# Performance work log

Hardware: AMD Instinct MI355X
Metric: run time of the kernel (lower is better)

Reference implementation:

```python
import jax, jax.numpy as jnp
import numpy as np

N, C, H, W = 10, 512, 40, 40
HW = H * W
OUT_CH = 128
EPS = 1e-12

def _l2norm(x, axis):
    # matches F.normalize: v / max(||v||_2, eps)
    n = jnp.sqrt(jnp.sum(x * x, axis=axis, keepdims=True))
    return x / jnp.maximum(n, EPS)

def _conv(x, w, b, pad):
    y = jax.lax.conv_general_dilated(
        x, w, window_strides=(1, 1), padding=[(pad, pad), (pad, pad)],
        dimension_numbers=('NCHW', 'OIHW', 'NCHW'))
    return y + b[None, :, None, None]

def setup_inputs() -> dict:
    key = jax.random.key(0)
    ks = jax.random.split(key, 6)
    feats = jax.random.normal(ks[0], (N, C, H, W), jnp.float32)
    SISMs = jax.random.uniform(ks[1], (N, 1, H, W), jnp.float32)
    # ResNetBlock(HW -> 128) params (Kaiming-uniform-ish fan-in bounds)
    s1 = float(1.0 / np.sqrt(HW * 9))
    s2 = float(1.0 / np.sqrt(OUT_CH * 9))
    ss = float(1.0 / np.sqrt(HW))
    w1 = jax.random.uniform(ks[2], (OUT_CH, HW, 3, 3), jnp.float32, -s1, s1)
    b1 = jnp.zeros((OUT_CH,), jnp.float32)
    w2 = jax.random.uniform(ks[3], (OUT_CH, OUT_CH, 3, 3), jnp.float32, -s2, s2)
    b2 = jnp.zeros((OUT_CH,), jnp.float32)
    ws = jax.random.uniform(ks[4], (OUT_CH, HW, 1, 1), jnp.float32, -ss, ss)
    bs = jnp.zeros((OUT_CH,), jnp.float32)
    return dict(feats=feats, SISMs=SISMs, w1=w1, b1=b1, w2=w2, b2=b2, ws=ws, bs=bs)

def reference(feats, SISMs, w1, b1, w2, b2, ws, bs):
    # SISMs supplied at (H,W): bilinear resize w/ align_corners=True at same size is identity
    NFs = _l2norm(feats, axis=1)                                   # (N,C,H,W)
    SIVs = _l2norm(jnp.mean(NFs * SISMs, axis=(-1, -2)), axis=1)   # (N,C)
    # CFM: 1x1 conv of NFs with SIVs as filters -> (N,N,H,W)
    cm = jnp.einsum('nchw,mc->nmhw', NFs, SIVs).reshape(N, N, HW)
    cm = _l2norm(cm, axis=2)
    corr = jnp.einsum('nmk,npk->nmp', cm, cm)                      # (N,N,N)
    wv = jax.nn.softmax(jnp.sum(corr, axis=2), axis=1)             # (N,N)
    CSA = jnp.sum(cm * wv[:, :, None], axis=1)                     # (N,HW)
    mn = jnp.min(CSA, axis=1, keepdims=True)
    mx = jnp.max(CSA, axis=1, keepdims=True)
    CSA = (CSA - mn) / (mx - mn + EPS)
    CSA_maps = CSA.reshape(N, 1, H, W)
    # self-correlation features: (N, HW, H, W)
    NFf = NFs.reshape(N, C, HW)
    SCFs = jnp.einsum('nci,ncj->nij', NFf, NFf).reshape(N, HW, H, W)
    # reorder channels by descending CSA evidence
    idx = jnp.argsort(-CSA, axis=1)                                # (N,HW)
    RSCFs = jnp.take_along_axis(SCFs, idx[:, :, None, None], axis=1)
    x = RSCFs * CSA_maps
    # ResNetBlock: relu(conv2(relu(conv1(x))) + shortcut_1x1(x))
    h = jax.nn.relu(_conv(x, w1, b1, 1))
    h = _conv(h, w2, b2, 1)
    sc = _conv(x, ws, bs, 0)
    return jax.nn.relu(h + sc)
```

## Files before the change

### kernel.cpp

```cpp
#include <hip/hip_runtime.h>
#include <hip/hip_bf16.h>
#include <math.h>

typedef short short8 __attribute__((ext_vector_type(8)));
typedef short short4v __attribute__((ext_vector_type(4)));
typedef float f32x4 __attribute__((ext_vector_type(4)));
typedef __hip_bfloat16 bf16;

#define KN 10
#define KC 512
#define KHW 1600
#define KH 40
#define KOC 128
#define KPW 42
#define KM 1280

__device__ __forceinline__ void gload16(const void* g, void* l) {
  __builtin_amdgcn_global_load_lds(
      (const __attribute__((address_space(1))) unsigned int*)g,
      (__attribute__((address_space(3))) unsigned int*)l, 16, 0, 0);
}

__device__ __forceinline__ double blockReduceSumD(double v) {
  __shared__ double tmpS[8];
  int lane = threadIdx.x & 63, wv = threadIdx.x >> 6;
  #pragma unroll
  for (int o = 32; o > 0; o >>= 1) v += __shfl_down(v, o);
  if (lane == 0) tmpS[wv] = v;
  __syncthreads();
  if (threadIdx.x == 0) {
    int nw = (blockDim.x + 63) >> 6;
    double s = 0;
    for (int i = 0; i < nw; i++) s += tmpS[i];
    tmpS[0] = s;
  }
  __syncthreads();
  double r = tmpS[0];
  __syncthreads();
  return r;
}

__device__ __forceinline__ double blockReduceMinD(double v) {
  __shared__ double tmpMn[8];
  int lane = threadIdx.x & 63, wv = threadIdx.x >> 6;
  #pragma unroll
  for (int o = 32; o > 0; o >>= 1) v = fmin(v, __shfl_down(v, o));
  if (lane == 0) tmpMn[wv] = v;
  __syncthreads();
  if (threadIdx.x == 0) {
    int nw = (blockDim.x + 63) >> 6;
    double s = tmpMn[0];
    for (int i = 1; i < nw; i++) s = fmin(s, tmpMn[i]);
    tmpMn[0] = s;
  }
  __syncthreads();
  double r = tmpMn[0];
  __syncthreads();
  return r;
}

__device__ __forceinline__ double blockReduceMaxD(double v) {
  __shared__ double tmpMx[8];
  int lane = threadIdx.x & 63, wv = threadIdx.x >> 6;
  #pragma unroll
  for (int o = 32; o > 0; o >>= 1) v = fmax(v, __shfl_down(v, o));
  if (lane == 0) tmpMx[wv] = v;
  __syncthreads();
  if (threadIdx.x == 0) {
    int nw = (blockDim.x + 63) >> 6;
    double s = tmpMx[0];
    for (int i = 1; i < nw; i++) s = fmax(s, tmpMx[i]);
    tmpMx[0] = s;
  }
  __syncthreads();
  double r = tmpMx[0];
  __syncthreads();
  return r;
}


__global__ void k_rnormp(const float* __restrict__ feats, double* __restrict__ ps) {
  int t = blockIdx.x * 256 + threadIdx.x;
  if (t >= KN * KHW) return;
  int ci = blockIdx.y;
  int n = t / KHW, k = t % KHW;
  const float* p = feats + (size_t)n * KC * KHW + (size_t)ci * 128 * KHW + k;
  double s = 0.0;
  for (int c = 0; c < 128; ++c) { double v = p[(size_t)c * KHW]; s += v * v; }
  ps[(size_t)ci * KN * KHW + t] = s;
}

__global__ void k_rnormc(const double* __restrict__ ps, double* __restrict__ rnorm) {
  int t = blockIdx.x * 256 + threadIdx.x;
  if (t >= KN * KHW) return;
  double s = ps[t] + ps[KN * KHW + t] + ps[2 * KN * KHW + t] + ps[3 * KN * KHW + t];
  double nn = sqrt(s);
  if (nn < 1e-12) nn = 1e-12;
  rnorm[t] = 1.0 / nn;
}

__global__ void k_nft(const float* __restrict__ feats, const double* __restrict__ rnorm,
                      const float* __restrict__ sism, bf16* __restrict__ NFT,
                      double* __restrict__ vpp) {
  __shared__ float T[32][33];
  int n = blockIdx.z, k0 = blockIdx.x * 32, c0 = blockIdx.y * 32;
  int tx = threadIdx.x, ty = threadIdx.y;
  const float* fb = feats + ((size_t)n * KC + c0) * KHW + k0;
  #pragma unroll
  for (int ii = 0; ii < 4; ii++) {
    int cl = ty * 4 + ii;
    T[cl][tx] = fb[(size_t)cl * KHW + tx];
  }
  __syncthreads();
  bf16* ob = NFT + ((size_t)n * KHW + k0) * KC + c0;
  #pragma unroll
  for (int ii = 0; ii < 4; ii++) {
    int kl = ty * 4 + ii;
    float r = (float)rnorm[n * KHW + k0 + kl];
    ob[(size_t)kl * KC + tx] = __float2bfloat16(T[tx][kl] * r);
  }
  double rs = rnorm[n * KHW + k0 + tx] * (double)sism[n * KHW + k0 + tx];
  #pragma unroll
  for (int ii = 0; ii < 4; ii++) {
    int cl = ty * 4 + ii;
    double v = (double)T[cl][tx] * rs;
    #pragma unroll
    for (int o = 16; o > 0; o >>= 1) v += __shfl_down(v, o, 32);
    if (tx == 0) vpp[((size_t)n * KC + c0 + cl) * 50 + k0 / 32] = v;
  }
}

__global__ void k_sivnorm2(const double* __restrict__ vpp, double* __restrict__ SIV) {
  int n = blockIdx.x, c = threadIdx.x;
  const double* p = vpp + ((size_t)n * KC + c) * 50;
  double acc = 0;
  #pragma unroll 5
  for (int j = 0; j < 50; j++) acc += p[j];
  acc /= (double)KHW;
  double s2 = blockReduceSumD(acc * acc);
  double nn = sqrt(s2);
  if (nn < 1e-12) nn = 1e-12;
  SIV[n * KC + c] = acc / nn;
}

__global__ void k_cmP(const float* __restrict__ feats, const double* __restrict__ SIV,
                      double* __restrict__ cmp) {
  __shared__ double sv[KN][64];
  int kc = blockIdx.x, ci = blockIdx.y, n = blockIdx.z;
  for (int t = threadIdx.x; t < KN * 64; t += 256) {
    int m = t / 64, c = t % 64;
    sv[m][c] = SIV[m * KC + ci * 64 + c];
  }
  __syncthreads();
  int k = kc * 256 + threadIdx.x;
  if (k >= KHW) return;
  const float* f = feats + ((size_t)n * KC + ci * 64) * KHW + k;
  double acc[KN];
  #pragma unroll
  for (int m = 0; m < KN; m++) acc[m] = 0.0;
  for (int c = 0; c < 64; ++c) {
    double fv = f[(size_t)c * KHW];
    #pragma unroll
    for (int m = 0; m < KN; m++) acc[m] += fv * sv[m][c];
  }
  const size_t str = (size_t)KN * KN * KHW;
  #pragma unroll
  for (int m = 0; m < KN; m++)
    cmp[(size_t)ci * str + ((size_t)n * KN + m) * KHW + k] = acc[m];
}

__global__ void k_cmB(const double* __restrict__ cmp, const double* __restrict__ rnorm,
                      double* __restrict__ cm) {
  size_t t = (size_t)blockIdx.x * 256 + threadIdx.x;
  if (t >= (size_t)KN * KN * KHW) return;
  int k = t % KHW;
  int n = (int)(t / ((size_t)KN * KHW));
  const size_t str = (size_t)KN * KN * KHW;
  double s = 0;
  #pragma unroll
  for (int ci = 0; ci < 8; ci++) s += cmp[ci * str + t];
  cm[t] = s * rnorm[n * KHW + k];
}

__global__ void k_cmnorm(double* __restrict__ cm) {
  double* row = cm + (size_t)blockIdx.x * KHW;
  double s = 0;
  for (int k = threadIdx.x; k < KHW; k += 256) { double v = row[k]; s += v * v; }
  s = blockReduceSumD(s);
  double nn = sqrt(s);
  if (nn < 1e-12) nn = 1e-12;
  double rn = 1.0 / nn;
  for (int k = threadIdx.x; k < KHW; k += 256) row[k] *= rn;
}

__global__ void k_st(const double* __restrict__ cm, double* __restrict__ tbuf) {
  int b = blockIdx.x;
  int n = b / KN, m = b % KN;
  const double* base = cm + (size_t)n * KN * KHW;
  double acc = 0;
  for (int k = threadIdx.x; k < KHW; k += 256) {
    double S = 0;
    #pragma unroll
    for (int mm = 0; mm < KN; mm++) S += base[(size_t)mm * KHW + k];
    acc += base[(size_t)m * KHW + k] * S;
  }
  acc = blockReduceSumD(acc);
  if (threadIdx.x == 0) tbuf[b] = acc;
}

__global__ void k_csa(const double* __restrict__ cm, const double* __restrict__ tbuf,
                      double* __restrict__ CSAd, float* __restrict__ CSAf) {
  __shared__ double w[KN];
  int n = blockIdx.x, tid = threadIdx.x;
  if (tid == 0) {
    double v[KN], mx = -1e300;
    #pragma unroll
    for (int m = 0; m < KN; m++) { v[m] = tbuf[n * KN + m]; mx = fmax(mx, v[m]); }
    double s = 0;
    #pragma unroll
    for (int m = 0; m < KN; m++) { v[m] = exp(v[m] - mx); s += v[m]; }
    #pragma unroll
    for (int m = 0; m < KN; m++) w[m] = v[m] / s;
  }
  __syncthreads();
  double v[7];
  int cnt = 0;
  double lmin = 1e300, lmax = -1e300;
  for (int k = tid; k < KHW; k += 256) {
    double a = 0;
    #pragma unroll
    for (int m = 0; m < KN; m++) a += cm[((size_t)n * KN + m) * KHW + k] * w[m];
    v[cnt++] = a;
    lmin = fmin(lmin, a);
    lmax = fmax(lmax, a);
  }
  double mn = blockReduceMinD(lmin);
  double mx = blockReduceMaxD(lmax);
  double inv = 1.0 / (mx - mn + 1e-12);
  cnt = 0;
  for (int k = tid; k < KHW; k += 256) {
    double nv = (v[cnt++] - mn) * inv;
    CSAd[(size_t)n * KHW + k] = nv;
    CSAf[(size_t)n * KHW + k] = (float)nv;
  }
}

__global__ void k_rank(const double* __restrict__ CSAd, int* __restrict__ idx) {
  __shared__ double key[KHW];
  int b = blockIdx.x;
  int n = b / 100, it = b % 100;
  const double* src = CSAd + (size_t)n * KHW;
  for (int j = threadIdx.x; j < KHW; j += 256) key[j] = src[j];
  __syncthreads();
  int wave = threadIdx.x >> 6, lane = threadIdx.x & 63;
  int i0 = it * 16 + wave * 4;
  double ki[4];
  #pragma unroll
  for (int ii = 0; ii < 4; ii++) ki[ii] = key[i0 + ii];
  int r[4] = {0, 0, 0, 0};
  #pragma unroll
  for (int q = 0; q < 25; q++) {
    int j = q * 64 + lane;
    double kj = key[j];
    #pragma unroll
    for (int ii = 0; ii < 4; ii++) {
      int i = i0 + ii;
      r[ii] += (kj > ki[ii]) || (kj == ki[ii] && j < i);
    }
  }
  #pragma unroll
  for (int ii = 0; ii < 4; ii++) {
    int v = r[ii];
    #pragma unroll
    for (int o = 32; o > 0; o >>= 1) v += __shfl_down(v, o);
    if (lane == 0) idx[n * KHW + v] = i0 + ii;
  }
}

__global__ void k_prepw1s(const float* __restrict__ w1, const float* __restrict__ wsc,
                          bf16* __restrict__ w1s) {
  int t = blockIdx.x * 256 + threadIdx.x;
  int m = t / KHW, i = t % KHW;
  int tau = m >> 7, o = m & 127;
  float v = (tau < 9) ? w1[((size_t)o * KHW + i) * 9 + tau]
                      : wsc[(size_t)o * KHW + i];
  w1s[t] = __float2bfloat16(v);
}

__global__ void k_prepw2(const float* __restrict__ w2, bf16* __restrict__ w2p) {
  int t = blockIdx.x * 256 + threadIdx.x;
  if (t >= KOC * 9 * KOC) return;
  int o = t / (9 * KOC), r = t % (9 * KOC);
  int s = r / KOC, i = r % KOC;
  w2p[t] = __float2bfloat16(w2[(size_t)o * 9 * KOC + (size_t)i * 9 + s]);
}

__global__ void k_gath2(const short* __restrict__ NFT, const int* __restrict__ idx,
                        short* __restrict__ NFcg) {
  __shared__ short T[32][33];
  int i0 = blockIdx.x * 32, c0 = blockIdx.y * 32, n = blockIdx.z;
  int tx = threadIdx.x, ty = threadIdx.y;
  #pragma unroll
  for (int ii = 0; ii < 4; ii++) {
    int row = ty * 4 + ii;
    int id = idx[n * KHW + i0 + row];
    T[row][tx] = NFT[((size_t)n * KHW + id) * KC + c0 + tx];
  }
  __syncthreads();
  #pragma unroll
  for (int ii = 0; ii < 4; ii++) {
    int cl = ty * 4 + ii;
    NFcg[((size_t)n * KC + c0 + cl) * KHW + i0 + tx] = T[tx][cl];
  }
}

__global__ void k_zprep(const bf16* __restrict__ NFT, const float* __restrict__ CSAf,
                        bf16* __restrict__ Zpad) {
  int t = blockIdx.x * 256 + threadIdx.x;
  const int per_n = KHW * (KC / 4);
  int n = t / per_n, r = t % per_n;
  int p = r / (KC / 4), cq = r % (KC / 4);
  float cs = CSAf[n * KHW + p];
  const short* src = (const short*)(NFT + ((size_t)n * KHW + p) * KC) + cq * 4;
  short4v v = *(const short4v*)src;
  short4v o;
  #pragma unroll
  for (int j = 0; j < 4; j++) {
    short s = v[j];
    bf16 hb = *reinterpret_cast<bf16*>(&s);
    bf16 res = __float2bfloat16(__bfloat162float(hb) * cs);
    o[j] = *reinterpret_cast<short*>(&res);
  }
  int y = p / KH, x = p % KH;
  short* dst = (short*)(Zpad + ((size_t)n * KPW * KPW + (size_t)(y + 1) * KPW + (x + 1)) * KC) + cq * 4;
  *(short4v*)dst = o;
}

__global__ __launch_bounds__(256) void k_gemmU(const short* __restrict__ w1s,
                                               const short* __restrict__ NFcg,
                                               bf16* __restrict__ Uc,
                                               bf16* __restrict__ Usc) {
  __shared__ __align__(16) short smem[8704];
  short* As = smem;
  short* Bs = smem + 2048;
  short* Cs = smem;
  int b = blockIdx.x;
  int workid = (b & 7) * 100 + (b >> 3);
  int pair = workid / 20;
  int th = workid % 20;
  int n = pair >> 2, c0 = (pair & 3) * 128;
  int tau = th >> 1, half = th & 1;
  int m0 = tau * 128 + half * 64;
  int tid = threadIdx.x, lane = tid & 63, wave = tid >> 6;
  int quad = lane >> 4, l15 = lane & 15;
  int wm = (wave & 1) * 32, wn = (wave >> 1) * 64;
  int ar = tid >> 2, ko = (tid & 3) * 8;
  const short* Bb = NFcg + (size_t)n * KC * KHW;
  const short* pa0 = w1s + (size_t)(m0 + ar) * KHW + ko;
  const short* pb0 = Bb + (size_t)(c0 + ar) * KHW + ko;
  const short* pb1 = Bb + (size_t)(c0 + ar + 64) * KHW + ko;
  char* dA  = (char*)As + tid * 16;
  char* dB0 = (char*)Bs + tid * 16;
  char* dB1 = (char*)Bs + 4096 + tid * 16;
  f32x4 acc[2][4] = {};
  for (int k0 = 0; k0 < KHW; k0 += 32) {
    __syncthreads();
    gload16(pa0 + k0, dA);
    gload16(pb0 + k0, dB0);
    gload16(pb1 + k0, dB1);
    __syncthreads();
    short8 a[2], bb[4];
    #pragma unroll
    for (int t = 0; t < 2; t++) a[t] = *(const short8*)&As[(wm + t * 16 + l15) * 32 + quad * 8];
    #pragma unroll
    for (int t = 0; t < 4; t++) bb[t] = *(const short8*)&Bs[(wn + t * 16 + l15) * 32 + quad * 8];
    #pragma unroll
    for (int ti = 0; ti < 2; ti++)
      #pragma unroll
      for (int tj = 0; tj < 4; tj++)
        acc[ti][tj] = __builtin_amdgcn_mfma_f32_16x16x32_bf16(a[ti], bb[tj], acc[ti][tj], 0, 0, 0);
  }
  __syncthreads();
  #pragma unroll
  for (int ti = 0; ti < 2; ti++) {
    int lr = wm + ti * 16 + quad * 4;
    #pragma unroll
    for (int tj = 0; tj < 4; tj++) {
      int lc = wn + tj * 16 + l15;
      #pragma unroll
      for (int r = 0; r < 4; r++)
        *(bf16*)&Cs[(lr + r) * 136 + lc] = __float2bfloat16(acc[ti][tj][r]);
    }
  }
  __syncthreads();
  int dyq = tau / 3, dxq = tau % 3;
  #pragma unroll
  for (int pass = 0; pass < 4; pass++) {
    int row = pass * 16 + (tid >> 4);
    int col = (tid & 15) * 8;
    if (tau < 9) {
      *(float4*)&Uc[((size_t)((n * 3 + dyq) * 128 + half * 64 + row)) * 1536 + dxq * 512 + c0 + col] =
          *(const float4*)&Cs[row * 136 + col];
    } else {
      *(float4*)&Usc[((size_t)(n * 128 + half * 64 + row)) * 512 + c0 + col] =
          *(const float4*)&Cs[row * 136 + col];
    }
  }
}

__global__ __launch_bounds__(256) void k_convh(const short* __restrict__ Uc,
                                               const short* __restrict__ Usc,
                                               const short* __restrict__ Zpad,
                                               float* __restrict__ Hpart) {
  __shared__ __align__(16) short smem[24576];
  short* As = smem;
  short* Bs = smem + 16384;
  int b = blockIdx.x;
  int wgid = (b & 7) * 125 + (b >> 3);
  int n = wgid / 100, rest = wgid % 100;
  int dy = rest / 25, pt = rest % 25;
  int p0 = pt * 64;
  int tid = threadIdx.x, lane = tid & 63, wave = tid >> 6;
  int quad = lane >> 4, l15 = lane & 15;
  int wm = (wave & 1) * 64, wn = (wave >> 1) * 32;
  int sk = ((tid & 7) ^ ((tid >> 3) & 7)) * 8;
  int rowg = tid >> 3;
  bool isconv = (dy < 3);
  const short* Zb = Zpad + (size_t)n * KPW * KPW * KC;
  const short* Abase = isconv ? Uc + ((size_t)((n * 3 + dy) * 128)) * 1536
                              : Usc + ((size_t)(n * 128)) * 512;
  int astr = isconv ? 1536 : 512;
  const short* pA[4];
  #pragma unroll
  for (int g = 0; g < 4; g++)
    pA[g] = Abase + (size_t)(g * 32 + rowg) * astr + sk;
  const short* pB[2];
  #pragma unroll
  for (int g = 0; g < 2; g++) {
    int p = p0 + g * 32 + rowg;
    int y = p / KH, x = p % KH;
    int yy = isconv ? (y + dy) : (y + 1);
    int xx = isconv ? x : (x + 1);
    pB[g] = Zb + ((size_t)yy * KPW + xx) * KC + sk;
  }
  char* lA = (char*)As + tid * 16;
  char* lB = (char*)Bs + tid * 16;
  int NS = isconv ? 24 : 8;
  int bq = (l15 >> 2) & 1;
  int qx = (quad ^ (l15 & 3)) * 8;
  int koff0 = 32 * bq + qx;
  int koff1 = 32 * (1 - bq) + qx;
  f32x4 acc[4][2] = {};
  gload16(pA[0], lA); gload16(pA[1], lA + 4096);
  gload16(pA[2], lA + 8192); gload16(pA[3], lA + 12288);
  gload16(pB[0], lB); gload16(pB[1], lB + 4096);
  for (int s = 0; s < NS; s++) {
    int cb = s & 1, nb = cb ^ 1;
    if (s + 1 < NS) {
      int off = (s + 1) * 64;
      char* la = lA + nb * 16384;
      char* lb = lB + nb * 8192;
      gload16(pA[0] + off, la); gload16(pA[1] + off, la + 4096);
      gload16(pA[2] + off, la + 8192); gload16(pA[3] + off, la + 12288);
      gload16(pB[0] + off, lb); gload16(pB[1] + off, lb + 4096);
      asm volatile("s_waitcnt vmcnt(6)" ::: "memory");
    } else {
      asm volatile("s_waitcnt vmcnt(0)" ::: "memory");
    }
    __builtin_amdgcn_s_barrier();
    __builtin_amdgcn_sched_barrier(0);
    const short* Ab = As + cb * 8192;
    const short* Bb = Bs + cb * 4096;
    #pragma unroll
    for (int ks = 0; ks < 2; ks++) {
      int ko = (ks == 0) ? koff0 : koff1;
      short8 av[4], bv[2];
      #pragma unroll
      for (int t = 0; t < 4; t++) av[t] = *(const short8*)&Ab[(wm + t * 16 + l15) * 64 + ko];
      #pragma unroll
      for (int t = 0; t < 2; t++) bv[t] = *(const short8*)&Bb[(wn + t * 16 + l15) * 64 + ko];
      #pragma unroll
      for (int ti = 0; ti < 4; ti++)
        #pragma unroll
        for (int tj = 0; tj < 2; tj++)
          acc[ti][tj] = __builtin_amdgcn_mfma_f32_16x16x32_bf16(av[ti], bv[tj], acc[ti][tj], 0, 0, 0);
    }
    __builtin_amdgcn_s_barrier();
  }
  float* cbp = Hpart + ((size_t)(dy * KN + n)) * KOC * KHW;
  #pragma unroll
  for (int ti = 0; ti < 4; ti++) {
    int o = wm + ti * 16 + quad * 4;
    #pragma unroll
    for (int tj = 0; tj < 2; tj++) {
      int q = p0 + wn + tj * 16 + l15;
      #pragma unroll
      for (int r = 0; r < 4; r++)
        cbp[(size_t)(o + r) * KHW + q] = acc[ti][tj][r];
    }
  }
}

__global__ void k_hprep3(const float* __restrict__ Hpart, const float* __restrict__ b1,
                         bf16* __restrict__ hpadT) {
  __shared__ float T[32][132];
  int n = blockIdx.y, p0 = blockIdx.x * 32;
  int tx = threadIdx.x, ty = threadIdx.y;
  const size_t str = (size_t)KN * KOC * KHW;
  const float* hb = Hpart + (size_t)n * KOC * KHW;
  #pragma unroll
  for (int oc = 0; oc < 16; oc++) {
    int o = oc * 8 + ty;
    size_t off = (size_t)o * KHW + p0 + tx;
    T[tx][o] = fmaxf(hb[off] + hb[str + off] + hb[2 * str + off] + b1[o], 0.0f);
  }
  __syncthreads();
  bf16* hp = hpadT + (size_t)n * KPW * KPW * KOC;
  #pragma unroll
  for (int pc = 0; pc < 4; pc++) {
    int pl = ty * 4 + pc;
    int pp = p0 + pl;
    int yy = pp / KH, xx = pp % KH;
    bf16* row = hp + ((size_t)(yy + 1) * KPW + (xx + 1)) * KOC;
    #pragma unroll
    for (int u = 0; u < 4; u++) row[tx * 4 + u] = __float2bfloat16(T[pl][tx * 4 + u]);
  }
}

__global__ __launch_bounds__(256) void k_conv2(const short* __restrict__ w2p,
                                               const short* __restrict__ hpadT,
                                               float* __restrict__ Cpart) {
  __shared__ __align__(16) short smem[24576];
  short* As = smem;
  short* Bs = smem + 16384;
  int b = blockIdx.x;
  int xcd = b & 7, bi = b >> 3;
  int wgid = (xcd < 6 ? xcd * 94 : 6 * 94 + (xcd - 6) * 93) + bi;
  int n = wgid / 75, rest = wgid % 75;
  int dy = rest / 25, pt = rest % 25;
  int p0 = pt * 64;
  int tid = threadIdx.x, lane = tid & 63, wave = tid >> 6;
  int quad = lane >> 4, l15 = lane & 15;
  int wm = (wave & 1) * 64, wn = (wave >> 1) * 32;
  int sk = ((tid & 7) ^ ((tid >> 3) & 7)) * 8;
  int rowg = tid >> 3;
  const short* hb = hpadT + (size_t)n * KPW * KPW * KOC;
  const short* pA[4];
  #pragma unroll
  for (int g = 0; g < 4; g++)
    pA[g] = w2p + (size_t)(g * 32 + rowg) * (9 * KOC) + dy * 384 + sk;
  const short* pB[2];
  #pragma unroll
  for (int g = 0; g < 2; g++) {
    int p = p0 + g * 32 + rowg;
    int y = p / KH, x = p % KH;
    pB[g] = hb + ((size_t)(y + dy) * KPW + x) * KOC + sk;
  }
  char* lA = (char*)As + tid * 16;
  char* lB = (char*)Bs + tid * 16;
  const int NS = 6;
  int bq = (l15 >> 2) & 1;
  int qx = (quad ^ (l15 & 3)) * 8;
  int koff0 = 32 * bq + qx;
  int koff1 = 32 * (1 - bq) + qx;
  f32x4 acc[4][2] = {};
  gload16(pA[0], lA); gload16(pA[1], lA + 4096);
  gload16(pA[2], lA + 8192); gload16(pA[3], lA + 12288);
  gload16(pB[0], lB); gload16(pB[1], lB + 4096);
  for (int s = 0; s < NS; s++) {
    int cb = s & 1, nb = cb ^ 1;
    if (s + 1 < NS) {
      int off = (s + 1) * 64;
      char* la = lA + nb * 16384;
      char* lb = lB + nb * 8192;
      gload16(pA[0] + off, la); gload16(pA[1] + off, la + 4096);
      gload16(pA[2] + off, la + 8192); gload16(pA[3] + off, la + 12288);
      gload16(pB[0] + off, lb); gload16(pB[1] + off, lb + 4096);
      asm volatile("s_waitcnt vmcnt(6)" ::: "memory");
    } else {
      asm volatile("s_waitcnt vmcnt(0)" ::: "memory");
    }
    __builtin_amdgcn_s_barrier();
    __builtin_amdgcn_sched_barrier(0);
    const short* Ab = As + cb * 8192;
    const short* Bb = Bs + cb * 4096;
    #pragma unroll
    for (int ks = 0; ks < 2; ks++) {
      int ko = (ks == 0) ? koff0 : koff1;
      short8 av[4], bv[2];
      #pragma unroll
      for (int t = 0; t < 4; t++) av[t] = *(const short8*)&Ab[(wm + t * 16 + l15) * 64 + ko];
      #pragma unroll
      for (int t = 0; t < 2; t++) bv[t] = *(const short8*)&Bb[(wn + t * 16 + l15) * 64 + ko];
      #pragma unroll
      for (int ti = 0; ti < 4; ti++)
        #pragma unroll
        for (int tj = 0; tj < 2; tj++)
          acc[ti][tj] = __builtin_amdgcn_mfma_f32_16x16x32_bf16(av[ti], bv[tj], acc[ti][tj], 0, 0, 0);
    }
    __builtin_amdgcn_s_barrier();
  }
  float* cbp = Cpart + ((size_t)(dy * KN + n)) * KOC * KHW;
  #pragma unroll
  for (int ti = 0; ti < 4; ti++) {
    int o = wm + ti * 16 + quad * 4;
    #pragma unroll
    for (int tj = 0; tj < 2; tj++) {
      int q = p0 + wn + tj * 16 + l15;
      #pragma unroll
      for (int r = 0; r < 4; r++)
        cbp[(size_t)(o + r) * KHW + q] = acc[ti][tj][r];
    }
  }
}

__global__ void k_final2(const float* __restrict__ Cpart, const float* __restrict__ Hpart,
                         const float* __restrict__ b2, const float* __restrict__ bs,
                         float* __restrict__ out) {
  int t = blockIdx.x * 256 + threadIdx.x;
  if (t >= KN * KOC * KHW) return;
  int o = (t / KHW) % KOC;
  const size_t stride = (size_t)KN * KOC * KHW;
  float v = Cpart[t] + Cpart[stride + t] + Cpart[2 * stride + t] +
            Hpart[3 * stride + t] + b2[o] + bs[o];
  out[t] = fmaxf(v, 0.0f);
}

extern "C" void kernel_launch(void* const* d_in, const int* in_sizes, int n_in,
                              void* d_out, int out_size, void* d_ws, size_t ws_size,
                              hipStream_t stream) {
  const float* feats = (const float*)d_in[0];
  const float* sisms = (const float*)d_in[1];
  const float* w1 = (const float*)d_in[2];
  const float* b1 = (const float*)d_in[3];
  const float* w2 = (const float*)d_in[4];
  const float* b2 = (const float*)d_in[5];
  const float* wsc = (const float*)d_in[6];
  const float* bsc = (const float*)d_in[7];
  float* out = (float*)d_out;

  char* w = (char*)d_ws;
  auto carve = [&](size_t bytes) -> void* {
    void* p = (void*)w;
    w += (bytes + 255) & ~(size_t)255;
    return p;
  };
  bf16* NFT   = (bf16*)carve((size_t)KN * KHW * KC * 2);
  bf16* NFcg  = (bf16*)carve((size_t)KN * KC * KHW * 2);
  bf16* Uc    = (bf16*)carve((size_t)KN * 3 * 128 * 1536 * 2);
  bf16* Usc   = (bf16*)carve((size_t)KN * 128 * 512 * 2);
  bf16* w1s   = (bf16*)carve((size_t)KM * KHW * 2);
  bf16* Zpad  = (bf16*)carve((size_t)KN * KPW * KPW * KC * 2);
  bf16* hpadT = (bf16*)carve((size_t)KN * KPW * KPW * KOC * 2);
  float* Hpart = (float*)carve((size_t)4 * KN * KOC * KHW * 4);
  float* Cpart = (float*)carve((size_t)3 * KN * KOC * KHW * 4);
  bf16* w2p   = (bf16*)carve((size_t)KOC * 9 * KOC * 2);
  double* psbuf = (double*)carve((size_t)4 * KN * KHW * 8);
  double* rnorm = (double*)carve((size_t)KN * KHW * 8);
  double* vpp   = (double*)carve((size_t)KN * KC * 50 * 8);
  double* SIV   = (double*)carve((size_t)KN * KC * 8);
  double* cmp   = (double*)carve((size_t)8 * KN * KN * KHW * 8);
  double* cm    = (double*)carve((size_t)KN * KN * KHW * 8);
  double* tbuf  = (double*)carve((size_t)KN * KN * 8);
  double* CSAd  = (double*)carve((size_t)KN * KHW * 8);
  float* CSAf   = (float*)carve((size_t)KN * KHW * 4);
  int* idxb     = (int*)carve((size_t)KN * KHW * 4);

  hipMemsetAsync(hpadT, 0, (size_t)KN * KPW * KPW * KOC * 2, stream);
  hipMemsetAsync(Zpad, 0, (size_t)KN * KPW * KPW * KC * 2, stream);

  k_rnormp<<<dim3(63, 4), 256, 0, stream>>>(feats, psbuf);
  k_rnormc<<<63, 256, 0, stream>>>(psbuf, rnorm);
  k_nft<<<dim3(50, 16, KN), dim3(32, 8), 0, stream>>>(feats, rnorm, sisms, NFT, vpp);
  k_sivnorm2<<<KN, 512, 0, stream>>>(vpp, SIV);
  k_cmP<<<dim3(7, 8, KN), 256, 0, stream>>>(feats, SIV, cmp);
  k_cmB<<<625, 256, 0, stream>>>(cmp, rnorm, cm);
  k_cmnorm<<<KN * KN, 256, 0, stream>>>(cm);
  k_st<<<KN * KN, 256, 0, stream>>>(cm, tbuf);
  k_csa<<<KN, 256, 0, stream>>>(cm, tbuf, CSAd, CSAf);
  k_rank<<<1000, 256, 0, stream>>>(CSAd, idxb);

  k_prepw1s<<<KM * KHW / 256, 256, 0, stream>>>(w1, wsc, w1s);
  k_prepw2<<<576, 256, 0, stream>>>(w2, w2p);
  k_gath2<<<dim3(50, 16, KN), dim3(32, 8), 0, stream>>>((const short*)NFT, idxb, (short*)NFcg);
  k_zprep<<<KN * KHW * (KC / 4) / 256, 256, 0, stream>>>(NFT, CSAf, Zpad);

  k_gemmU<<<800, 256, 0, stream>>>((const short*)w1s, (const short*)NFcg, Uc, Usc);
  k_convh<<<1000, 256, 0, stream>>>((const short*)Uc, (const short*)Usc,
                                    (const short*)Zpad, Hpart);
  k_hprep3<<<dim3(50, KN), dim3(32, 8), 0, stream>>>(Hpart, b1, hpadT);
  k_conv2<<<750, 256, 0, stream>>>((const short*)w2p, (const short*)hpadT, Cpart);
  k_final2<<<8000, 256, 0, stream>>>(Cpart, Hpart, b2, bsc, out);
}
```

Measured before the change: 301.4 us.

## Double-buffer k_gemmU LDS tiles with K=64 steps and XOR swizzle

Result: faster. 285.5 us (-5.3%).

```diff
diff --git a/kernel.cpp b/kernel.cpp
--- a/kernel.cpp
+++ b/kernel.cpp
@@ -340,9 +340,9 @@
                                                const short* __restrict__ NFcg,
                                                bf16* __restrict__ Uc,
                                                bf16* __restrict__ Usc) {
-  __shared__ __align__(16) short smem[8704];
+  __shared__ __align__(16) short smem[24576];
   short* As = smem;
-  short* Bs = smem + 2048;
+  short* Bs = smem + 8192;
   short* Cs = smem;
   int b = blockIdx.x;
   int workid = (b & 7) * 100 + (b >> 3);
@@ -354,33 +354,61 @@
   int tid = threadIdx.x, lane = tid & 63, wave = tid >> 6;
   int quad = lane >> 4, l15 = lane & 15;
   int wm = (wave & 1) * 32, wn = (wave >> 1) * 64;
-  int ar = tid >> 2, ko = (tid & 3) * 8;
+  int sk = ((tid & 7) ^ ((tid >> 3) & 7)) * 8;
+  int rowg = tid >> 3;
   const short* Bb = NFcg + (size_t)n * KC * KHW;
-  const short* pa0 = w1s + (size_t)(m0 + ar) * KHW + ko;
-  const short* pb0 = Bb + (size_t)(c0 + ar) * KHW + ko;
-  const short* pb1 = Bb + (size_t)(c0 + ar + 64) * KHW + ko;
-  char* dA  = (char*)As + tid * 16;
-  char* dB0 = (char*)Bs + tid * 16;
-  char* dB1 = (char*)Bs + 4096 + tid * 16;
+  const short* pA[2];
+  #pragma unroll
+  for (int g = 0; g < 2; g++)
+    pA[g] = w1s + (size_t)(m0 + g * 32 + rowg) * KHW + sk;
+  const short* pB[4];
+  #pragma unroll
+  for (int g = 0; g < 4; g++)
+    pB[g] = Bb + (size_t)(c0 + g * 32 + rowg) * KHW + sk;
+  char* lA = (char*)As + tid * 16;
+  char* lB = (char*)Bs + tid * 16;
+  int bq = (l15 >> 2) & 1;
+  int qx = (quad ^ (l15 & 3)) * 8;
+  int koff0 = 32 * bq + qx;
+  int koff1 = 32 * (1 - bq) + qx;
   f32x4 acc[2][4] = {};
-  for (int k0 = 0; k0 < KHW; k0 += 32) {
-    __syncthreads();
-    gload16(pa0 + k0, dA);
-    gload16(pb0 + k0, dB0);
-    gload16(pb1 + k0, dB1);
-    __syncthreads();
-    short8 a[2], bb[4];
-    #pragma unroll
-    for (int t = 0; t < 2; t++) a[t] = *(const short8*)&As[(wm + t * 16 + l15) * 32 + quad * 8];
-    #pragma unroll
-    for (int t = 0; t < 4; t++) bb[t] = *(const short8*)&Bs[(wn + t * 16 + l15) * 32 + quad * 8];
-    #pragma unroll
-    for (int ti = 0; ti < 2; ti++)
-      #pragma unroll
-      for (int tj = 0; tj < 4; tj++)
-        acc[ti][tj] = __builtin_amdgcn_mfma_f32_16x16x32_bf16(a[ti], bb[tj], acc[ti][tj], 0, 0, 0);
-  }
-  __syncthreads();
+  gload16(pA[0], lA); gload16(pA[1], lA + 4096);
+  gload16(pB[0], lB); gload16(pB[1], lB + 4096);
+  gload16(pB[2], lB + 8192); gload16(pB[3], lB + 12288);
+  const int NS = 25;
+  for (int s = 0; s < NS; s++) {
+    int cb = s & 1, nb = cb ^ 1;
+    if (s + 1 < NS) {
+      int off = (s + 1) * 64;
+      char* la = lA + nb * 8192;
+      char* lb = lB + nb * 16384;
+      gload16(pA[0] + off, la); gload16(pA[1] + off, la + 4096);
+      gload16(pB[0] + off, lb); gload16(pB[1] + off, lb + 4096);
+      gload16(pB[2] + off, lb + 8192); gload16(pB[3] + off, lb + 12288);
+      asm volatile("s_waitcnt vmcnt(6)" ::: "memory");
+    } else {
+      asm volatile("s_waitcnt vmcnt(0)" ::: "memory");
+    }
+    __builtin_amdgcn_s_barrier();
+    __builtin_amdgcn_sched_barrier(0);
+    const short* Ab = As + cb * 4096;
+    const short* Bbf = Bs + cb * 8192;
+    #pragma unroll
+    for (int ks = 0; ks < 2; ks++) {
+      int ko = (ks == 0) ? koff0 : koff1;
+      short8 av[2], bv[4];
+      #pragma unroll
+      for (int t = 0; t < 2; t++) av[t] = *(const short8*)&Ab[(wm + t * 16 + l15) * 64 + ko];
+      #pragma unroll
+      for (int t = 0; t < 4; t++) bv[t] = *(const short8*)&Bbf[(wn + t * 16 + l15) * 64 + ko];
+      #pragma unroll
+      for (int ti = 0; ti < 2; ti++)
+        #pragma unroll
+        for (int tj = 0; tj < 4; tj++)
+          acc[ti][tj] = __builtin_amdgcn_mfma_f32_16x16x32_bf16(av[ti], bv[tj], acc[ti][tj], 0, 0, 0);
+    }
+    __builtin_amdgcn_s_barrier();
+  }
   #pragma unroll
   for (int ti = 0; ti < 2; ti++) {
     int lr = wm + ti * 16 + quad * 4;
```
